# Performance work log

Hardware: AMD Instinct MI355X
Metric: run time of the kernel (lower is better)

Reference implementation:

```python
import jax, jax.numpy as jnp
import numpy as np

B, T, O, D, H, EA, R, NB = 64, 90, 5, 256, 256, 4096, 5, 8
NPG = T + O          # nodes per graph
N = B * NPG          # total nodes


def setup_inputs() -> dict:
    key = jax.random.key(0)
    ks = jax.random.split(key, 11)
    M = jax.random.normal(ks[0], (B, T, D), jnp.float32)            # r_out proxy
    x = jax.random.normal(ks[1], (N, D), jnp.float32)               # graph_input nodes
    node_att = jax.random.uniform(ks[2], (B, T, O), jnp.float32)    # softmax(f_predicts) proxy
    edge_src = jax.random.randint(ks[3], (B, EA), 0, T, jnp.int32)
    edge_dst = jax.random.randint(ks[4], (B, EA), 0, T, jnp.int32)
    edge_type = jax.random.randint(ks[5], (B, EA), 0, R, jnp.int32)
    Ws = jax.random.normal(ks[6], (T, D), jnp.float32) / np.float32(np.sqrt(D))       # EdgeAttention.scalar (max_seq_len x D)
    bases = jax.random.normal(ks[7], (NB, D, H), jnp.float32) / np.float32(np.sqrt(D))  # RGCN basis weights
    comp = jax.random.normal(ks[8], (R, NB), jnp.float32) / np.float32(np.sqrt(NB))
    root = jax.random.normal(ks[9], (D, H), jnp.float32) / np.float32(np.sqrt(D))
    bias = jnp.zeros((H,), jnp.float32)
    return dict(M=M, x=x, node_att=node_att, Ws=Ws, bases=bases, comp=comp,
                root=root, bias=bias, edge_src=edge_src, edge_dst=edge_dst,
                edge_type=edge_type)


def reference(M, x, node_att, Ws, bases, comp, root, bias, edge_src, edge_dst, edge_type):
    # ---- EdgeAttention: scale = Linear(M)[:, :, :T]; softmax over dim=1; permute(0,2,1) ----
    scale = jnp.einsum('btd,sd->bts', M, Ws)[:, :, :T]        # [B,T,T]
    alpha = jax.nn.softmax(scale, axis=1).transpose(0, 2, 1)  # [B,T,T]

    # ---- edge_norm gather: scores[b, src, dst] for attention edges, node_att for tag edges ----
    b_idx = jnp.arange(B)[:, None]
    norm_att = alpha[b_idx, edge_src, edge_dst]               # [B,EA]
    norm_tag = node_att.reshape(B, T * O)                     # node_att[b].view(-1)
    edge_norm = jnp.concatenate([norm_att, norm_tag], axis=1).reshape(-1)  # [E]

    # ---- build block-diagonal batched edge index (tag edges: utt i -> user node T+o) ----
    tag_src = jnp.broadcast_to(jnp.repeat(jnp.arange(T, dtype=jnp.int32), O), (B, T * O))
    tag_dst = jnp.broadcast_to(T + jnp.tile(jnp.arange(O, dtype=jnp.int32), T), (B, T * O))
    src_l = jnp.concatenate([edge_src, tag_src], axis=1)
    dst_l = jnp.concatenate([edge_dst, tag_dst], axis=1)
    et = jnp.concatenate([edge_type, jnp.full((B, T * O), R - 1, jnp.int32)], axis=1)
    offset = (jnp.arange(B, dtype=jnp.int32) * NPG)[:, None]
    src = (src_l + offset).reshape(-1)                        # [E] global src
    dst = (dst_l + offset).reshape(-1)                        # [E] global dst
    et = et.reshape(-1)                                       # [E]

    # ---- basis-decomposed RGCN: msg_e = edge_norm_e * (x[src_e] @ W[type_e]) ----
    W = jnp.einsum('rn,ndh->rdh', comp, bases)                # [R,D,H]
    x_e = x[src]                                              # [E,D] irregular gather
    msg = jnp.zeros((src.shape[0], H), x.dtype)
    for r in range(R):                                        # loop over few relations (structural)
        msg = msg + jnp.where((et == r)[:, None], x_e @ W[r], jnp.zeros((), x.dtype))
    msg = msg * edge_norm[:, None]
    agg = jax.ops.segment_sum(msg, dst, num_segments=N)       # scatter-add at dst
    out = agg + x @ root + bias                               # self/root transform + bias
    return out.reshape(B, NPG, H)                             # graph_out.view(B, T+O, -1)
```

## Files before the change

kernel.cpp:

```cpp
#include <hip/hip_runtime.h>
#include <cstddef>
#include <cstdint>

#define Bq 64
#define Tq 90
#define Oq 5
#define Dq 256
#define Hq 256
#define EAq 4096
#define Rq 5
#define NBq 8
#define NPGq 95

typedef __attribute__((ext_vector_type(8))) short bf16x8;
typedef __attribute__((ext_vector_type(8))) unsigned short u16x8;
typedef __attribute__((ext_vector_type(4))) float f32x4;
typedef __attribute__((address_space(1))) const unsigned int gu32;
typedef __attribute__((address_space(3))) unsigned int lu32;

__device__ __forceinline__ unsigned short f2bf(float f) {
    unsigned u = __float_as_uint(f);
    unsigned r = (u + 0x7FFF + ((u >> 16) & 1)) >> 16;
    return (unsigned short)r;
}
__device__ __forceinline__ float bf2f(unsigned short s) {
    return __uint_as_float(((unsigned)s) << 16);
}

__global__ __launch_bounds__(256) void k_wt(const float* __restrict__ bases,
                                            const float* __restrict__ comp,
                                            const float* __restrict__ rootw,
                                            unsigned short* __restrict__ Wt) {
    __shared__ float Ld[32][257];
    int wblk = blockIdx.x;
    int rs = wblk >> 3;
    int d0 = (wblk & 7) * 32;
    int t = threadIdx.x;
    float cmp[NBq];
    if (rs < Rq)
#pragma unroll
        for (int nb = 0; nb < NBq; ++nb) cmp[nb] = comp[rs * NBq + nb];
    for (int dl = 0; dl < 32; ++dl) {
        int d = d0 + dl;
        float v;
        if (rs < Rq) {
            v = 0.f;
#pragma unroll
            for (int nb = 0; nb < NBq; ++nb)
                v += cmp[nb] * bases[((size_t)nb * Dq + d) * Hq + t];
        } else {
            v = rootw[(size_t)d * Hq + t];
        }
        Ld[dl][t] = v;
    }
    __syncthreads();
    int c = t & 31, hg = t >> 5;
    for (int hh = 0; hh < 32; ++hh) {
        int h = hg * 32 + hh;
        Wt[(size_t)(rs * 256 + h) * Dq + d0 + c] = f2bf(Ld[c][h]);
    }
}

__global__ __launch_bounds__(576) void k_fused(const float* __restrict__ M,
                                               const float* __restrict__ Ws,
                                               const float* __restrict__ natt,
                                               const int* __restrict__ esrc,
                                               const int* __restrict__ edst,
                                               const int* __restrict__ etype,
                                               const float* __restrict__ x,
                                               const unsigned short* __restrict__ Wt,
                                               const float* __restrict__ bias,
                                               float* __restrict__ out) {
    __shared__ __attribute__((aligned(16))) char lds[137984];
    unsigned short* Mb = (unsigned short*)lds;
    unsigned short* Wb = (unsigned short*)(lds + 49152);
    float* P   = (float*)lds;
    float* mxs = (float*)(lds + 137216);
    float* rds = (float*)(lds + 137600);
    char* const Xs   = lds;
    char* const Wl   = lds + 49152;
    float* const Acc = (float*)(lds + 81920);
    char* const Ztl  = lds + 81920;
    char* const A2l  = lds + 118784;

    const int tid = threadIdx.x;
    const int w = tid >> 6, l = tid & 63;
    const int b  = blockIdx.x & 63;
    const int hc = blockIdx.x >> 6;

    int es[8], ed[8], et[8];
#pragma unroll
    for (int k = 0; k < 8; ++k) {
        int j = tid + k * 576;
        if (j < EAq) {
            es[k] = esrc[(size_t)b * EAq + j];
            ed[k] = edst[(size_t)b * EAq + j];
            et[k] = etype[(size_t)b * EAq + j];
        }
    }
    float tagv = (tid < Tq * Oq) ? natt[(size_t)b * (Tq * Oq) + tid] : 0.f;

#pragma unroll
    for (int i = 0; i < 6; ++i) {
        int idx = tid + i * 576;
        if (idx < 3072) {
            int row = idx >> 5, c = idx & 31;
            u16x8 pm, pw;
            if (row < Tq) {
                const float4* ms = (const float4*)(M + ((size_t)b * Tq + row) * Dq + c * 8);
                float4 a0 = ms[0], a1 = ms[1];
                pm[0] = f2bf(a0.x); pm[1] = f2bf(a0.y); pm[2] = f2bf(a0.z); pm[3] = f2bf(a0.w);
                pm[4] = f2bf(a1.x); pm[5] = f2bf(a1.y); pm[6] = f2bf(a1.z); pm[7] = f2bf(a1.w);
                const float4* ws = (const float4*)(Ws + (size_t)row * Dq + c * 8);
                float4 w0 = ws[0], w1 = ws[1];
                pw[0] = f2bf(w0.x); pw[1] = f2bf(w0.y); pw[2] = f2bf(w0.z); pw[3] = f2bf(w0.w);
                pw[4] = f2bf(w1.x); pw[5] = f2bf(w1.y); pw[6] = f2bf(w1.z); pw[7] = f2bf(w1.w);
            } else {
#pragma unroll
                for (int q = 0; q < 8; ++q) { pm[q] = 0; pw[q] = 0; }
            }
            int off = row * 512 + ((c * 16) ^ ((row & 7) << 4));
            *(u16x8*)((char*)Mb + off) = pm;
            *(u16x8*)((char*)Wb + off) = pw;
        }
    }
    __syncthreads();

    {
        const int wr = w / 3, wc = w % 3;
        f32x4 pacc[2][2];
#pragma unroll
        for (int i = 0; i < 2; ++i)
#pragma unroll
            for (int j = 0; j < 2; ++j) pacc[i][j] = (f32x4)0.0f;
#pragma unroll
        for (int ks = 0; ks < 8; ++ks) {
            int kb = ks * 64 + (l >> 4) * 16;
            bf16x8 af[2], bfv[2];
#pragma unroll
            for (int mi = 0; mi < 2; ++mi) {
                int row = wr * 32 + mi * 16 + (l & 15);
                af[mi] = *(const bf16x8*)((char*)Mb + row * 512 + (kb ^ ((row & 7) << 4)));
            }
#pragma unroll
            for (int ni = 0; ni < 2; ++ni) {
                int row = wc * 32 + ni * 16 + (l & 15);
                bfv[ni] = *(const bf16x8*)((char*)Wb + row * 512 + (kb ^ ((row & 7) << 4)));
            }
#pragma unroll
            for (int mi = 0; mi < 2; ++mi)
#pragma unroll
                for (int ni = 0; ni < 2; ++ni)
                    pacc[mi][ni] = __builtin_amdgcn_mfma_f32_16x16x32_bf16(
                        af[mi], bfv[ni], pacc[mi][ni], 0, 0, 0);
        }
        __syncthreads();

#pragma unroll
        for (int mi = 0; mi < 2; ++mi)
#pragma unroll
            for (int ni = 0; ni < 2; ++ni)
#pragma unroll
                for (int j = 0; j < 4; ++j) {
                    int rowp = wr * 32 + mi * 16 + (l >> 4) * 4 + j;
                    int colp = wc * 32 + ni * 16 + (l & 15);
                    P[rowp * 97 + colp] = pacc[mi][ni][j];
                }
    }
    __syncthreads();

    if (tid < 96) {
        float m = -1e30f;
        for (int t = 0; t < Tq; ++t) m = fmaxf(m, P[t * 97 + tid]);
        float s = 0.f;
        for (int t = 0; t < Tq; ++t) s += __expf(P[t * 97 + tid] - m);
        mxs[tid] = m;
        rds[tid] = 1.f / s;
    }
    __syncthreads();

    float v[8];
#pragma unroll
    for (int k = 0; k < 8; ++k) {
        int j = tid + k * 576;
        if (j < EAq)
            v[k] = __expf(P[ed[k] * 97 + es[k]] - mxs[es[k]]) * rds[es[k]];
    }
    __syncthreads();

#pragma unroll
    for (int i = 0; i < 6; ++i) {
        int idx = tid + i * 576;
        if (idx < 3072) {
            int row = idx >> 5, c = idx & 31;
            u16x8 pk;
            if (row < NPGq) {
                const float4* xs4 = (const float4*)(x + ((size_t)b * NPGq + row) * Dq + c * 8);
                float4 a = xs4[0], b2 = xs4[1];
                pk[0] = f2bf(a.x);  pk[1] = f2bf(a.y);  pk[2] = f2bf(a.z);  pk[3] = f2bf(a.w);
                pk[4] = f2bf(b2.x); pk[5] = f2bf(b2.y); pk[6] = f2bf(b2.z); pk[7] = f2bf(b2.w);
            } else {
#pragma unroll
                for (int q = 0; q < 8; ++q) pk[q] = 0;
            }
            *(u16x8*)(Xs + row * 512 + ((c * 16) ^ ((row & 7) << 4))) = pk;
        }
    }

    auto stageW = [&](int slice) {
        int kkbase = slice * 256 + hc * 64;
#pragma unroll
        for (int i = 0; i < 4; ++i) {
            int idx = i * 576 + tid;
            if (idx < 2048) {
                int hrow = idx >> 5, c = idx & 31;
                const unsigned short* g = Wt + (size_t)(kkbase + hrow) * Dq + (c ^ (hrow & 7)) * 8;
                __builtin_amdgcn_global_load_lds((gu32*)g,
                    (lu32*)(unsigned int)(uintptr_t)(Wl + idx * 16), 16, 0, 0);
            }
        }
    };
    const int wrz = w >> 1, wcz = w & 1;
    const int wrn = w >> 2, wcn = w & 3;
    auto gemmZ = [&](f32x4 (&zacc)[3]) {
#pragma unroll
        for (int i = 0; i < 3; ++i) zacc[i] = (f32x4)0.0f;
#pragma unroll
        for (int ks = 0; ks < 8; ++ks) {
            int kb = ks * 64 + (l >> 4) * 16;
            int hl = wrz * 16 + (l & 15);
            bf16x8 af = *(const bf16x8*)(Wl + hl * 512 + (kb ^ ((hl & 7) << 4)));
#pragma unroll
            for (int ni = 0; ni < 3; ++ni) {
                int s = wcz * 48 + ni * 16 + (l & 15);
                bf16x8 xv = *(const bf16x8*)(Xs + s * 512 + (kb ^ ((s & 7) << 4)));
                zacc[ni] = __builtin_amdgcn_mfma_f32_16x16x32_bf16(af, xv, zacc[ni], 0, 0, 0);
            }
        }
    };
    auto writeZt = [&](f32x4 (&zacc)[3]) {
#pragma unroll
        for (int ni = 0; ni < 3; ++ni)
#pragma unroll
            for (int j = 0; j < 4; ++j) {
                int h = wrz * 16 + (l >> 4) * 4 + j;
                int s = wcz * 48 + ni * 16 + (l & 15);
                *(unsigned short*)(Ztl + h * 192 + (((s >> 3) ^ (h & 3)) << 4) + (s & 7) * 2)
                    = f2bf(zacc[ni][j]);
            }
    };

    stageW(0);
    __syncthreads();

    f32x4 acc[3];
#pragma unroll
    for (int i = 0; i < 3; ++i) acc[i] = (f32x4)0.0f;

    for (int r = 0; r < Rq; ++r) {
#pragma unroll
        for (int i = 0; i < 4; ++i)
            ((float4*)Acc)[tid + i * 576] = make_float4(0.f, 0.f, 0.f, 0.f);
        __syncthreads();
#pragma unroll
        for (int k = 0; k < 8; ++k) {
            int j = tid + k * 576;
            if (j < EAq && et[k] == r)
                atomicAdd(&Acc[ed[k] * 96 + es[k]], v[k]);
        }
        if (r == Rq - 1 && tid < Tq * Oq) {
            int t = tid / Oq, o = tid % Oq;
            Acc[(Tq + o) * 96 + t] = tagv;
        }
        __syncthreads();
#pragma unroll
        for (int i = 0; i < 2; ++i) {
            int c0 = tid + i * 576;
            int row = c0 / 12, u = c0 - row * 12;
            const float* src = Acc + row * 96 + u * 8;
            u16x8 pk;
#pragma unroll
            for (int q = 0; q < 8; ++q) pk[q] = f2bf(src[q]);
            *(u16x8*)(A2l + row * 192 + ((u ^ (row & 3)) << 4)) = pk;
        }
        __syncthreads();
        f32x4 zacc[3];
        if (w < 8) gemmZ(zacc);
        __syncthreads();
        stageW(r + 1);
        if (w < 8) writeZt(zacc);
        __syncthreads();
        if (w < 8) {
#pragma unroll
            for (int ks = 0; ks < 3; ++ks) {
                int kb = ks * 64 + (l >> 4) * 16;
                int h = wcn * 16 + (l & 15);
                bf16x8 bfv = *(const bf16x8*)(Ztl + h * 192 + (kb ^ ((h & 3) << 4)));
#pragma unroll
                for (int mi = 0; mi < 3; ++mi) {
                    int nl = wrn * 48 + mi * 16 + (l & 15);
                    bf16x8 af = *(const bf16x8*)(A2l + nl * 192 + (kb ^ ((nl & 3) << 4)));
                    acc[mi] = __builtin_amdgcn_mfma_f32_16x16x32_bf16(af, bfv, acc[mi], 0, 0, 0);
                }
            }
        }
        __syncthreads();
    }

    f32x4 zacc[3];
    if (w < 8) gemmZ(zacc);
    if (w < 8) writeZt(zacc);
    __syncthreads();
    if (w < 8) {
        int h = wcn * 16 + (l & 15);
        float bv = bias[hc * 64 + h];
#pragma unroll
        for (int mi = 0; mi < 3; ++mi) {
#pragma unroll
            for (int j = 0; j < 4; ++j) {
                int nl = wrn * 48 + mi * 16 + (l >> 4) * 4 + j;
                float rv = bf2f(*(const unsigned short*)(Ztl + h * 192 +
                                (((nl >> 3) ^ (h & 3)) << 4) + (nl & 7) * 2));
                if (nl < NPGq)
                    out[((size_t)b * NPGq + nl) * Hq + hc * 64 + h] = acc[mi][j] + rv + bv;
            }
        }
    }
}

extern "C" void kernel_launch(void* const* d_in, const int* in_sizes, int n_in,
                              void* d_out, int out_size, void* d_ws, size_t ws_size,
                              hipStream_t stream) {
    (void)in_sizes; (void)n_in; (void)out_size; (void)ws_size;
    const float* M     = (const float*)d_in[0];
    const float* x     = (const float*)d_in[1];
    const float* natt  = (const float*)d_in[2];
    const float* Ws    = (const float*)d_in[3];
    const float* bases = (const float*)d_in[4];
    const float* comp  = (const float*)d_in[5];
    const float* rootw = (const float*)d_in[6];
    const float* bias  = (const float*)d_in[7];
    const int* esrc    = (const int*)d_in[8];
    const int* edst    = (const int*)d_in[9];
    const int* etype   = (const int*)d_in[10];
    float* out = (float*)d_out;
    char* ws = (char*)d_ws;

    unsigned short* Wt = (unsigned short*)(ws + 0);

    k_wt<<<dim3(48), 256, 0, stream>>>(bases, comp, rootw, Wt);
    k_fused<<<dim3(256), 576, 0, stream>>>(M, Ws, natt, esrc, edst, etype,
                                           x, Wt, bias, out);
}
```

Baseline: 47.71 us.

## Merge kernels into cooperative launch and split attention work from GEMM blocks

Replaces the two-kernel launch with one cooperative kernel. Blocks 0-63 compute the attention softmax and the per-relation adjacency matrices once per graph and write them to global memory in bf16. Blocks 64-111 build the combined weights, and the remaining blocks stage x, all before a grid-wide sync. After the sync, every block runs the relation loop with double-buffered weight tiles and loads the adjacency rows through async global-to-LDS copies. This removes the attention work that was repeated four times per graph and one kernel launch, at the cost of a grid barrier, extra global round-trips, and load imbalance before the sync.

```diff
diff --git a/kernel.cpp b/kernel.cpp
--- a/kernel.cpp
+++ b/kernel.cpp
@@ -1,6 +1,9 @@
 #include <hip/hip_runtime.h>
+#include <hip/hip_cooperative_groups.h>
 #include <cstddef>
 #include <cstdint>
+
+namespace cg = cooperative_groups;
 
 #define Bq 64
 #define Tq 90
@@ -11,6 +14,7 @@
 #define Rq 5
 #define NBq 8
 #define NPGq 95
+#define KAq 480
 
 typedef __attribute__((ext_vector_type(8))) short bf16x8;
 typedef __attribute__((ext_vector_type(8))) unsigned short u16x8;
@@ -27,187 +31,233 @@
     return __uint_as_float(((unsigned)s) << 16);
 }
 
-__global__ __launch_bounds__(256) void k_wt(const float* __restrict__ bases,
-                                            const float* __restrict__ comp,
-                                            const float* __restrict__ rootw,
-                                            unsigned short* __restrict__ Wt) {
-    __shared__ float Ld[32][257];
-    int wblk = blockIdx.x;
-    int rs = wblk >> 3;
-    int d0 = (wblk & 7) * 32;
-    int t = threadIdx.x;
-    float cmp[NBq];
-    if (rs < Rq)
-#pragma unroll
-        for (int nb = 0; nb < NBq; ++nb) cmp[nb] = comp[rs * NBq + nb];
-    for (int dl = 0; dl < 32; ++dl) {
-        int d = d0 + dl;
-        float v;
-        if (rs < Rq) {
-            v = 0.f;
-#pragma unroll
-            for (int nb = 0; nb < NBq; ++nb)
-                v += cmp[nb] * bases[((size_t)nb * Dq + d) * Hq + t];
-        } else {
-            v = rootw[(size_t)d * Hq + t];
-        }
-        Ld[dl][t] = v;
-    }
-    __syncthreads();
-    int c = t & 31, hg = t >> 5;
-    for (int hh = 0; hh < 32; ++hh) {
-        int h = hg * 32 + hh;
-        Wt[(size_t)(rs * 256 + h) * Dq + d0 + c] = f2bf(Ld[c][h]);
-    }
-}
-
-__global__ __launch_bounds__(576) void k_fused(const float* __restrict__ M,
-                                               const float* __restrict__ Ws,
-                                               const float* __restrict__ natt,
-                                               const int* __restrict__ esrc,
-                                               const int* __restrict__ edst,
-                                               const int* __restrict__ etype,
-                                               const float* __restrict__ x,
-                                               const unsigned short* __restrict__ Wt,
-                                               const float* __restrict__ bias,
-                                               float* __restrict__ out) {
-    __shared__ __attribute__((aligned(16))) char lds[137984];
+__global__ __launch_bounds__(576) void k_all(const float* __restrict__ M,
+                                             const float* __restrict__ Ws,
+                                             const float* __restrict__ natt,
+                                             const int* __restrict__ esrc,
+                                             const int* __restrict__ edst,
+                                             const int* __restrict__ etype,
+                                             const float* __restrict__ x,
+                                             const float* __restrict__ bases,
+                                             const float* __restrict__ comp,
+                                             const float* __restrict__ rootw,
+                                             const float* __restrict__ bias,
+                                             unsigned short* __restrict__ A2b,
+                                             unsigned short* __restrict__ Wt,
+                                             float* __restrict__ out) {
+    __shared__ __attribute__((aligned(16))) char lds[145408];
     unsigned short* Mb = (unsigned short*)lds;
     unsigned short* Wb = (unsigned short*)(lds + 49152);
     float* P   = (float*)lds;
+    float* Acc = (float*)(lds + 49152);
     float* mxs = (float*)(lds + 137216);
     float* rds = (float*)(lds + 137600);
-    char* const Xs   = lds;
-    char* const Wl   = lds + 49152;
-    float* const Acc = (float*)(lds + 81920);
-    char* const Ztl  = lds + 81920;
-    char* const A2l  = lds + 118784;
+    char* const Xs  = lds;
+    char* const Wl0 = lds + 49152;
+    char* const Wl1 = lds + 81920;
+    char* const Ztl = lds + 114688;
+    char* const A2l = lds + 126976;
 
     const int tid = threadIdx.x;
     const int w = tid >> 6, l = tid & 63;
-    const int b  = blockIdx.x & 63;
-    const int hc = blockIdx.x >> 6;
-
-    int es[8], ed[8], et[8];
-#pragma unroll
-    for (int k = 0; k < 8; ++k) {
-        int j = tid + k * 576;
-        if (j < EAq) {
-            es[k] = esrc[(size_t)b * EAq + j];
-            ed[k] = edst[(size_t)b * EAq + j];
-            et[k] = etype[(size_t)b * EAq + j];
-        }
+    const int blk = blockIdx.x;
+    const int b  = blk & 63;
+    const int hc = blk >> 6;
+
+    auto stageXs = [&]() {
+#pragma unroll
+        for (int i = 0; i < 6; ++i) {
+            int idx = tid + i * 576;
+            if (idx < 3072) {
+                int row = idx >> 5, c = idx & 31;
+                u16x8 pk;
+                if (row < NPGq) {
+                    const float4* xs4 = (const float4*)(x + ((size_t)b * NPGq + row) * Dq + c * 8);
+                    float4 a = xs4[0], b2 = xs4[1];
+                    pk[0] = f2bf(a.x);  pk[1] = f2bf(a.y);  pk[2] = f2bf(a.z);  pk[3] = f2bf(a.w);
+                    pk[4] = f2bf(b2.x); pk[5] = f2bf(b2.y); pk[6] = f2bf(b2.z); pk[7] = f2bf(b2.w);
+                } else {
+#pragma unroll
+                    for (int q = 0; q < 8; ++q) pk[q] = 0;
+                }
+                *(u16x8*)(Xs + row * 512 + ((c * 16) ^ ((row & 7) << 4))) = pk;
+            }
+        }
+    };
+
+    if (blk < 64) {
+        int es[8], ed[8], et[8];
+#pragma unroll
+        for (int k = 0; k < 8; ++k) {
+            int j = tid + k * 576;
+            if (j < EAq) {
+                es[k] = esrc[(size_t)b * EAq + j];
+                ed[k] = edst[(size_t)b * EAq + j];
+                et[k] = etype[(size_t)b * EAq + j];
+            }
+        }
+        float tagv = (tid < Tq * Oq) ? natt[(size_t)b * (Tq * Oq) + tid] : 0.f;
+
+#pragma unroll
+        for (int i = 0; i < 6; ++i) {
+            int idx = tid + i * 576;
+            if (idx < 3072) {
+                int row = idx >> 5, c = idx & 31;
+                u16x8 pm, pw;
+                if (row < Tq) {
+                    const float4* ms = (const float4*)(M + ((size_t)b * Tq + row) * Dq + c * 8);
+                    float4 a0 = ms[0], a1 = ms[1];
+                    pm[0] = f2bf(a0.x); pm[1] = f2bf(a0.y); pm[2] = f2bf(a0.z); pm[3] = f2bf(a0.w);
+                    pm[4] = f2bf(a1.x); pm[5] = f2bf(a1.y); pm[6] = f2bf(a1.z); pm[7] = f2bf(a1.w);
+                    const float4* ws = (const float4*)(Ws + (size_t)row * Dq + c * 8);
+                    float4 w0 = ws[0], w1 = ws[1];
+                    pw[0] = f2bf(w0.x); pw[1] = f2bf(w0.y); pw[2] = f2bf(w0.z); pw[3] = f2bf(w0.w);
+                    pw[4] = f2bf(w1.x); pw[5] = f2bf(w1.y); pw[6] = f2bf(w1.z); pw[7] = f2bf(w1.w);
+                } else {
+#pragma unroll
+                    for (int q = 0; q < 8; ++q) { pm[q] = 0; pw[q] = 0; }
+                }
+                int off = row * 512 + ((c * 16) ^ ((row & 7) << 4));
+                *(u16x8*)((char*)Mb + off) = pm;
+                *(u16x8*)((char*)Wb + off) = pw;
+            }
+        }
+        __syncthreads();
+
+        {
+            const int wr = w / 3, wc = w % 3;
+            f32x4 pacc[2][2];
+#pragma unroll
+            for (int i = 0; i < 2; ++i)
+#pragma unroll
+                for (int j = 0; j < 2; ++j) pacc[i][j] = (f32x4)0.0f;
+#pragma unroll
+            for (int ks = 0; ks < 8; ++ks) {
+                int kb = ks * 64 + (l >> 4) * 16;
+                bf16x8 af[2], bfv[2];
+#pragma unroll
+                for (int mi = 0; mi < 2; ++mi) {
+                    int row = wr * 32 + mi * 16 + (l & 15);
+                    af[mi] = *(const bf16x8*)((char*)Mb + row * 512 + (kb ^ ((row & 7) << 4)));
+                }
+#pragma unroll
+                for (int ni = 0; ni < 2; ++ni) {
+                    int row = wc * 32 + ni * 16 + (l & 15);
+                    bfv[ni] = *(const bf16x8*)((char*)Wb + row * 512 + (kb ^ ((row & 7) << 4)));
+                }
+#pragma unroll
+                for (int mi = 0; mi < 2; ++mi)
+#pragma unroll
+                    for (int ni = 0; ni < 2; ++ni)
+                        pacc[mi][ni] = __builtin_amdgcn_mfma_f32_16x16x32_bf16(
+                            af[mi], bfv[ni], pacc[mi][ni], 0, 0, 0);
+            }
+            __syncthreads();
+
+#pragma unroll
+            for (int mi = 0; mi < 2; ++mi)
+#pragma unroll
+                for (int ni = 0; ni < 2; ++ni)
+#pragma unroll
+                    for (int j = 0; j < 4; ++j) {
+                        int rowp = wr * 32 + mi * 16 + (l >> 4) * 4 + j;
+                        int colp = wc * 32 + ni * 16 + (l & 15);
+                        P[rowp * 97 + colp] = pacc[mi][ni][j];
+                    }
+        }
+        __syncthreads();
+
+        if (tid < 96) {
+            float m = -1e30f;
+            for (int t = 0; t < Tq; ++t) m = fmaxf(m, P[t * 97 + tid]);
+            float s = 0.f;
+            for (int t = 0; t < Tq; ++t) s += __expf(P[t * 97 + tid] - m);
+            mxs[tid] = m;
+            rds[tid] = 1.f / s;
+        }
+        __syncthreads();
+
+        float v[8];
+#pragma unroll
+        for (int k = 0; k < 8; ++k) {
+            int j = tid + k * 576;
+            if (j < EAq)
+                v[k] = __expf(P[ed[k] * 97 + es[k]] - mxs[es[k]]) * rds[es[k]];
+        }
+
+        for (int r = 0; r < Rq; ++r) {
+#pragma unroll
+            for (int i = 0; i < 4; ++i)
+                ((float4*)Acc)[tid + i * 576] = make_float4(0.f, 0.f, 0.f, 0.f);
+            __syncthreads();
+#pragma unroll
+            for (int k = 0; k < 8; ++k) {
+                int j = tid + k * 576;
+                if (j < EAq && et[k] == r)
+                    atomicAdd(&Acc[ed[k] * 96 + es[k]], v[k]);
+            }
+            if (r == Rq - 1 && tid < Tq * Oq) {
+                int t = tid / Oq, o = tid % Oq;
+                Acc[(Tq + o) * 96 + t] = tagv;
+            }
+            __syncthreads();
+#pragma unroll
+            for (int i = 0; i < 2; ++i) {
+                int c0 = tid + i * 576;
+                const float* src = Acc + (c0 / 12) * 96 + (c0 % 12) * 8;
+                u16x8 pk;
+#pragma unroll
+                for (int q = 0; q < 8; ++q) pk[q] = f2bf(src[q]);
+                *(u16x8*)(A2b + ((size_t)b * 96 + c0 / 12) * KAq + r * 96 + (c0 % 12) * 8) = pk;
+            }
+            __syncthreads();
+        }
+    } else if (blk < 112) {
+        float* Ld = (float*)lds;
+        int wblk = blk - 64;
+        int rs = wblk >> 3;
+        int d0 = (wblk & 7) * 32;
+        int t = tid;
+        if (t < 256) {
+            float cmp[NBq];
+            if (rs < Rq)
+#pragma unroll
+                for (int nb = 0; nb < NBq; ++nb) cmp[nb] = comp[rs * NBq + nb];
+            for (int dl = 0; dl < 32; ++dl) {
+                int d = d0 + dl;
+                float val;
+                if (rs < Rq) {
+                    val = 0.f;
+#pragma unroll
+                    for (int nb = 0; nb < NBq; ++nb)
+                        val += cmp[nb] * bases[((size_t)nb * Dq + d) * Hq + t];
+                } else {
+                    val = rootw[(size_t)d * Hq + t];
+                }
+                Ld[dl * 257 + t] = val;
+            }
+        }
+        __syncthreads();
+        if (t < 256) {
+            int c = t & 31, hg = t >> 5;
+            for (int hh = 0; hh < 32; ++hh) {
+                int h = hg * 32 + hh;
+                Wt[(size_t)(rs * 256 + h) * Dq + d0 + c] = f2bf(Ld[c * 257 + h]);
+            }
+        }
+    } else {
+        stageXs();
     }
-    float tagv = (tid < Tq * Oq) ? natt[(size_t)b * (Tq * Oq) + tid] : 0.f;
-
-#pragma unroll
-    for (int i = 0; i < 6; ++i) {
-        int idx = tid + i * 576;
-        if (idx < 3072) {
-            int row = idx >> 5, c = idx & 31;
-            u16x8 pm, pw;
-            if (row < Tq) {
-                const float4* ms = (const float4*)(M + ((size_t)b * Tq + row) * Dq + c * 8);
-                float4 a0 = ms[0], a1 = ms[1];
-                pm[0] = f2bf(a0.x); pm[1] = f2bf(a0.y); pm[2] = f2bf(a0.z); pm[3] = f2bf(a0.w);
-                pm[4] = f2bf(a1.x); pm[5] = f2bf(a1.y); pm[6] = f2bf(a1.z); pm[7] = f2bf(a1.w);
-                const float4* ws = (const float4*)(Ws + (size_t)row * Dq + c * 8);
-                float4 w0 = ws[0], w1 = ws[1];
-                pw[0] = f2bf(w0.x); pw[1] = f2bf(w0.y); pw[2] = f2bf(w0.z); pw[3] = f2bf(w0.w);
-                pw[4] = f2bf(w1.x); pw[5] = f2bf(w1.y); pw[6] = f2bf(w1.z); pw[7] = f2bf(w1.w);
-            } else {
-#pragma unroll
-                for (int q = 0; q < 8; ++q) { pm[q] = 0; pw[q] = 0; }
-            }
-            int off = row * 512 + ((c * 16) ^ ((row & 7) << 4));
-            *(u16x8*)((char*)Mb + off) = pm;
-            *(u16x8*)((char*)Wb + off) = pw;
-        }
-    }
-    __syncthreads();
-
-    {
-        const int wr = w / 3, wc = w % 3;
-        f32x4 pacc[2][2];
-#pragma unroll
-        for (int i = 0; i < 2; ++i)
-#pragma unroll
-            for (int j = 0; j < 2; ++j) pacc[i][j] = (f32x4)0.0f;
-#pragma unroll
-        for (int ks = 0; ks < 8; ++ks) {
-            int kb = ks * 64 + (l >> 4) * 16;
-            bf16x8 af[2], bfv[2];
-#pragma unroll
-            for (int mi = 0; mi < 2; ++mi) {
-                int row = wr * 32 + mi * 16 + (l & 15);
-                af[mi] = *(const bf16x8*)((char*)Mb + row * 512 + (kb ^ ((row & 7) << 4)));
-            }
-#pragma unroll
-            for (int ni = 0; ni < 2; ++ni) {
-                int row = wc * 32 + ni * 16 + (l & 15);
-                bfv[ni] = *(const bf16x8*)((char*)Wb + row * 512 + (kb ^ ((row & 7) << 4)));
-            }
-#pragma unroll
-            for (int mi = 0; mi < 2; ++mi)
-#pragma unroll
-                for (int ni = 0; ni < 2; ++ni)
-                    pacc[mi][ni] = __builtin_amdgcn_mfma_f32_16x16x32_bf16(
-                        af[mi], bfv[ni], pacc[mi][ni], 0, 0, 0);
-        }
-        __syncthreads();
-
-#pragma unroll
-        for (int mi = 0; mi < 2; ++mi)
-#pragma unroll
-            for (int ni = 0; ni < 2; ++ni)
-#pragma unroll
-                for (int j = 0; j < 4; ++j) {
-                    int rowp = wr * 32 + mi * 16 + (l >> 4) * 4 + j;
-                    int colp = wc * 32 + ni * 16 + (l & 15);
-                    P[rowp * 97 + colp] = pacc[mi][ni][j];
-                }
-    }
-    __syncthreads();
-
-    if (tid < 96) {
-        float m = -1e30f;
-        for (int t = 0; t < Tq; ++t) m = fmaxf(m, P[t * 97 + tid]);
-        float s = 0.f;
-        for (int t = 0; t < Tq; ++t) s += __expf(P[t * 97 + tid] - m);
-        mxs[tid] = m;
-        rds[tid] = 1.f / s;
-    }
-    __syncthreads();
-
-    float v[8];
-#pragma unroll
-    for (int k = 0; k < 8; ++k) {
-        int j = tid + k * 576;
-        if (j < EAq)
-            v[k] = __expf(P[ed[k] * 97 + es[k]] - mxs[es[k]]) * rds[es[k]];
-    }
-    __syncthreads();
-
-#pragma unroll
-    for (int i = 0; i < 6; ++i) {
-        int idx = tid + i * 576;
-        if (idx < 3072) {
-            int row = idx >> 5, c = idx & 31;
-            u16x8 pk;
-            if (row < NPGq) {
-                const float4* xs4 = (const float4*)(x + ((size_t)b * NPGq + row) * Dq + c * 8);
-                float4 a = xs4[0], b2 = xs4[1];
-                pk[0] = f2bf(a.x);  pk[1] = f2bf(a.y);  pk[2] = f2bf(a.z);  pk[3] = f2bf(a.w);
-                pk[4] = f2bf(b2.x); pk[5] = f2bf(b2.y); pk[6] = f2bf(b2.z); pk[7] = f2bf(b2.w);
-            } else {
-#pragma unroll
-                for (int q = 0; q < 8; ++q) pk[q] = 0;
-            }
-            *(u16x8*)(Xs + row * 512 + ((c * 16) ^ ((row & 7) << 4))) = pk;
-        }
-    }
-
-    auto stageW = [&](int slice) {
+
+    __threadfence();
+    cg::this_grid().sync();
+
+    if (blk < 112) stageXs();
+
+    const int wrz = w >> 1, wcz = w & 1;
+    const int wrn = w >> 2, wcn = w & 3;
+
+    auto stageW = [&](char* Wbuf, int slice) {
         int kkbase = slice * 256 + hc * 64;
 #pragma unroll
         for (int i = 0; i < 4; ++i) {
@@ -216,20 +266,29 @@
                 int hrow = idx >> 5, c = idx & 31;
                 const unsigned short* g = Wt + (size_t)(kkbase + hrow) * Dq + (c ^ (hrow & 7)) * 8;
                 __builtin_amdgcn_global_load_lds((gu32*)g,
-                    (lu32*)(unsigned int)(uintptr_t)(Wl + idx * 16), 16, 0, 0);
-            }
-        }
-    };
-    const int wrz = w >> 1, wcz = w & 1;
-    const int wrn = w >> 2, wcn = w & 3;
-    auto gemmZ = [&](f32x4 (&zacc)[3]) {
+                    (lu32*)(unsigned int)(uintptr_t)(Wbuf + idx * 16), 16, 0, 0);
+            }
+        }
+    };
+    auto stageA2 = [&](int r) {
+#pragma unroll
+        for (int i = 0; i < 2; ++i) {
+            int idx = i * 576 + tid;
+            int row = idx / 12, u = idx - row * 12;
+            int usw = u ^ (row & 3);
+            const unsigned short* g = A2b + ((size_t)b * 96 + row) * KAq + r * 96 + usw * 8;
+            __builtin_amdgcn_global_load_lds((gu32*)g,
+                (lu32*)(unsigned int)(uintptr_t)(A2l + idx * 16), 16, 0, 0);
+        }
+    };
+    auto gemmZ = [&](char* Wbuf, f32x4 (&zacc)[3]) {
 #pragma unroll
         for (int i = 0; i < 3; ++i) zacc[i] = (f32x4)0.0f;
 #pragma unroll
         for (int ks = 0; ks < 8; ++ks) {
             int kb = ks * 64 + (l >> 4) * 16;
             int hl = wrz * 16 + (l & 15);
-            bf16x8 af = *(const bf16x8*)(Wl + hl * 512 + (kb ^ ((hl & 7) << 4)));
+            bf16x8 af = *(const bf16x8*)(Wbuf + hl * 512 + (kb ^ ((hl & 7) << 4)));
 #pragma unroll
             for (int ni = 0; ni < 3; ++ni) {
                 int s = wcz * 48 + ni * 16 + (l & 15);
@@ -250,49 +309,25 @@
             }
     };
 
-    stageW(0);
+    stageW(Wl0, 0);
+    stageA2(0);
     __syncthreads();
 
     f32x4 acc[3];
 #pragma unroll
     for (int i = 0; i < 3; ++i) acc[i] = (f32x4)0.0f;
 
+    char* Wcur = Wl0;
+    char* Wnxt = Wl1;
     for (int r = 0; r < Rq; ++r) {
-#pragma unroll
-        for (int i = 0; i < 4; ++i)
-            ((float4*)Acc)[tid + i * 576] = make_float4(0.f, 0.f, 0.f, 0.f);
-        __syncthreads();
-#pragma unroll
-        for (int k = 0; k < 8; ++k) {
-            int j = tid + k * 576;
-            if (j < EAq && et[k] == r)
-                atomicAdd(&Acc[ed[k] * 96 + es[k]], v[k]);
-        }
-        if (r == Rq - 1 && tid < Tq * Oq) {
-            int t = tid / Oq, o = tid % Oq;
-            Acc[(Tq + o) * 96 + t] = tagv;
-        }
-        __syncthreads();
-#pragma unroll
-        for (int i = 0; i < 2; ++i) {
-            int c0 = tid + i * 576;
-            int row = c0 / 12, u = c0 - row * 12;
-            const float* src = Acc + row * 96 + u * 8;
-            u16x8 pk;
-#pragma unroll
-            for (int q = 0; q < 8; ++q) pk[q] = f2bf(src[q]);
-            *(u16x8*)(A2l + row * 192 + ((u ^ (row & 3)) << 4)) = pk;
-        }
-        __syncthreads();
         f32x4 zacc[3];
-        if (w < 8) gemmZ(zacc);
-        __syncthreads();
-        stageW(r + 1);
+        if (w < 8) gemmZ(Wcur, zacc);
+        stageW(Wnxt, r + 1);
         if (w < 8) writeZt(zacc);
         __syncthreads();
-        if (w < 8) {
-#pragma unroll
-            for (int ks = 0; ks < 3; ++ks) {
+#pragma unroll
+        for (int ks = 0; ks < 3; ++ks) {
+            if (w < 8) {
                 int kb = ks * 64 + (l >> 4) * 16;
                 int h = wcn * 16 + (l & 15);
                 bf16x8 bfv = *(const bf16x8*)(Ztl + h * 192 + (kb ^ ((h & 3) << 4)));
@@ -305,10 +340,12 @@
             }
         }
         __syncthreads();
+        if (r < Rq - 1) stageA2(r + 1);
+        char* t2 = Wcur; Wcur = Wnxt; Wnxt = t2;
     }
 
     f32x4 zacc[3];
-    if (w < 8) gemmZ(zacc);
+    if (w < 8) gemmZ(Wcur, zacc);
     if (w < 8) writeZt(zacc);
     __syncthreads();
     if (w < 8) {
@@ -346,9 +383,11 @@
     float* out = (float*)d_out;
     char* ws = (char*)d_ws;
 
-    unsigned short* Wt = (unsigned short*)(ws + 0);
-
-    k_wt<<<dim3(48), 256, 0, stream>>>(bases, comp, rootw, Wt);
-    k_fused<<<dim3(256), 576, 0, stream>>>(M, Ws, natt, esrc, edst, etype,
-                                           x, Wt, bias, out);
+    unsigned short* Wt  = (unsigned short*)(ws + 0);
+    unsigned short* A2b = (unsigned short*)(ws + 786432);
+
+    void* args[] = {(void*)&M, (void*)&Ws, (void*)&natt, (void*)&esrc, (void*)&edst,
+                    (void*)&etype, (void*)&x, (void*)&bases, (void*)&comp, (void*)&rootw,
+                    (void*)&bias, (void*)&A2b, (void*)&Wt, (void*)&out};
+    hipLaunchCooperativeKernel((const void*)k_all, dim3(256), dim3(576), args, 0, stream);
 }
```

Result: slower. 128.0 us (+168.3%).
